# Optimization experiments

Measured on AMD Instinct MI355X. Metric: run time of the kernel, lower is better.

Reference implementation:

```python
import jax, jax.numpy as jnp
import numpy as np

N_NODES = 100000


def _mean_agg(x, src, dst, n_nodes):
    # gather source features along edges, segment-sum into destinations, divide by in-degree
    msg = x[src]                                               # [E, D]
    s = jax.ops.segment_sum(msg, dst, num_segments=n_nodes)    # [N, D]
    deg = jax.ops.segment_sum(jnp.ones((src.shape[0],), x.dtype), dst, num_segments=n_nodes)
    return s / jnp.maximum(deg, 1.0)[:, None]


def _sage_layer(x, src, dst, W_self, W_neigh, b, n_nodes):
    h_neigh = _mean_agg(x, src, dst, n_nodes)
    return x @ W_self + h_neigh @ W_neigh + b


def setup_inputs() -> dict:
    key = jax.random.key(0)
    ks = jax.random.split(key, 8)
    in_f, h_f, n_cls = 128, 128, 40
    n_edges = 1600000
    sc = lambda d: 1.0 / np.sqrt(d)
    return {
        "features": jax.random.normal(ks[0], (N_NODES, in_f), dtype=jnp.float32),
        "src": jax.random.randint(ks[1], (n_edges,), 0, N_NODES),
        "dst": jax.random.randint(ks[2], (n_edges,), 0, N_NODES),
        "W1_self": jax.random.normal(ks[3], (in_f, h_f), dtype=jnp.float32) * sc(in_f),
        "W1_neigh": jax.random.normal(ks[4], (in_f, h_f), dtype=jnp.float32) * sc(in_f),
        "b1": jnp.zeros((h_f,), dtype=jnp.float32),
        "W2_self": jax.random.normal(ks[5], (h_f, n_cls), dtype=jnp.float32) * sc(h_f),
        "W2_neigh": jax.random.normal(ks[6], (h_f, n_cls), dtype=jnp.float32) * sc(h_f),
        "b2": jnp.zeros((n_cls,), dtype=jnp.float32),
    }


def reference(features, src, dst, W1_self, W1_neigh, b1, W2_self, W2_neigh, b2):
    h = _sage_layer(features, src, dst, W1_self, W1_neigh, b1, N_NODES)
    h = jax.nn.relu(h)
    h = _sage_layer(h, src, dst, W2_self, W2_neigh, b2, N_NODES)
    return h
```

## Files before the change

kernel.cpp:

```cpp
#include <hip/hip_runtime.h>


typedef __attribute__((ext_vector_type(8))) short bf16x8;
typedef __attribute__((ext_vector_type(4))) float f32x4;
typedef __attribute__((ext_vector_type(2))) float f32x2;

#define BIN_SHIFT 7
#define BIN_SIZE  128
#define NB        256

#define OFF_ROWSTART (1ull << 20)
#define OFF_HIST     (2ull << 20)
#define OFF_SCAN     (3ull << 20)
#define OFF_BSUMS    (4ull << 20)
#define OFF_BOFFS    ((4ull << 20) + (64ull << 10))
#define OFF_PACKED   (5ull << 20)
#define OFF_CSR      (12ull << 20)
#define OFF_W1T      (19ull << 20)
#define OFF_W2T      (20ull << 20)
#define OFF_XB       (21ull << 20)
#define OFF_XQ       (47ull << 20)
#define OFF_AGGB     (61ull << 20)
#define OFF_T2LO     (87ull << 20)
#define OFF_T2HI     (94ull << 20)

static __device__ __forceinline__ unsigned short f2b(float f) {
    unsigned int u = __float_as_uint(f);
    u += 0x7fffu + ((u >> 16) & 1u);
    return (unsigned short)(u >> 16);
}
static __device__ __forceinline__ float blo(unsigned int v) { return __uint_as_float(v << 16); }
static __device__ __forceinline__ float bhi(unsigned int v) { return __uint_as_float(v & 0xffff0000u); }


__global__ __launch_bounds__(256) void hist_local(
    const int* __restrict__ dst, int* __restrict__ hist, int E, int nbins) {
    __shared__ int h[1024];
    int b = blockIdx.x, t = threadIdx.x;
    for (int i = t; i < nbins; i += 256) h[i] = 0;
    __syncthreads();
    int chunk = (E + NB - 1) / NB;
    int base = b * chunk;
    int lim = min(base + chunk, E);
    for (int e = base + t; e < lim; e += 256)
        atomicAdd(&h[dst[e] >> BIN_SHIFT], 1);
    __syncthreads();
    for (int i = t; i < nbins; i += 256)
        hist[i * NB + b] = h[i];
}

__global__ void scan1(const int* __restrict__ in, int* __restrict__ tmp,
                      int* __restrict__ bsums, int M) {
    __shared__ int s[256];
    int t = threadIdx.x;
    int i = blockIdx.x * 256 + t;
    int v = (i < M) ? in[i] : 0;
    s[t] = v;
    __syncthreads();
    for (int off = 1; off < 256; off <<= 1) {
        int u = (t >= off) ? s[t - off] : 0;
        __syncthreads();
        s[t] += u;
        __syncthreads();
    }
    if (i < M) tmp[i] = s[t] - v;
    if (t == 255) bsums[blockIdx.x] = s[t];
}

__global__ void scan2(const int* __restrict__ bsums, int* __restrict__ boffs, int nb) {
    __shared__ int s[1024];
    int t = threadIdx.x;
    int v = (t < nb) ? bsums[t] : 0;
    s[t] = v;
    __syncthreads();
    for (int off = 1; off < 1024; off <<= 1) {
        int u = (t >= off) ? s[t - off] : 0;
        __syncthreads();
        s[t] += u;
        __syncthreads();
    }
    if (t < nb) boffs[t] = s[t] - v;
}

__global__ __launch_bounds__(256) void scatter_det(
    const int* __restrict__ src, const int* __restrict__ dst,
    const int* __restrict__ tmp, const int* __restrict__ boffs,
    unsigned int* __restrict__ packed, int E, int nbins) {
    __shared__ int cur[1024];
    int b = blockIdx.x, t = threadIdx.x;
    for (int i = t; i < nbins; i += 256) cur[i] = tmp[i * NB + b] + boffs[i];
    __syncthreads();
    int chunk = (E + NB - 1) / NB;
    int base = b * chunk;
    int lim = min(base + chunk, E);
    for (int e = base + t; e < lim; e += 256) {
        int d = dst[e];
        int bin = d >> BIN_SHIFT;
        int pos = atomicAdd(&cur[bin], 1);
        packed[pos] = ((unsigned int)(d & (BIN_SIZE - 1)) << 20) | (unsigned int)src[e];
    }
}

__global__ __launch_bounds__(256) void bin_fill(
    const unsigned int* __restrict__ packed, const int* __restrict__ tmp,
    const int* __restrict__ boffs,
    int* __restrict__ row_start, int* __restrict__ csr_src, int N, int nbins, int E) {
    __shared__ int cnt[BIN_SIZE];
    __shared__ int pre[BIN_SIZE];
    __shared__ int ex[BIN_SIZE];
    int b = blockIdx.x;
    int t = threadIdx.x;
    int node0 = b << BIN_SHIFT;
    int beg = tmp[b * NB] + boffs[b];
    int end = (b + 1 < nbins) ? (tmp[(b + 1) * NB] + boffs[b + 1]) : E;

    if (t < BIN_SIZE) cnt[t] = 0;
    __syncthreads();
    for (int i = beg + t; i < end; i += 256)
        atomicAdd(&cnt[packed[i] >> 20], 1);
    __syncthreads();
    if (t < BIN_SIZE) pre[t] = cnt[t];
    __syncthreads();
    for (int off = 1; off < BIN_SIZE; off <<= 1) {
        int u = (t < BIN_SIZE && t >= off) ? pre[t - off] : 0;
        __syncthreads();
        if (t < BIN_SIZE) pre[t] += u;
        __syncthreads();
    }
    if (t < BIN_SIZE) {
        ex[t] = pre[t] - cnt[t];
        int node = node0 + t;
        if (node < N) row_start[node] = beg + ex[t];
        cnt[t] = 0;
    }
    if (b == nbins - 1 && t == 0) row_start[N] = E;
    __syncthreads();
    for (int i = beg + t; i < end; i += 256) {
        unsigned int p = packed[i];
        int dl = p >> 20;
        int s = p & 0xFFFFF;
        int ofs = atomicAdd(&cnt[dl], 1);
        csr_src[beg + ex[dl] + ofs] = s;
    }
}


__global__ void cast_prep(const float* __restrict__ x,
                          const float* __restrict__ W1s, const float* __restrict__ W1n,
                          const float* __restrict__ W2s, const float* __restrict__ W2n,
                          unsigned short* __restrict__ xb, unsigned char* __restrict__ xq,
                          unsigned short* __restrict__ W1t, unsigned short* __restrict__ W2t,
                          unsigned short* __restrict__ t2lo, unsigned short* __restrict__ t2hi,
                          int n16, int castBlocks, int N) {
    int blk = blockIdx.x, t = threadIdx.x;
    if (blk < castBlocks) {
        int i = blk * 256 + t;
        if (i >= n16) return;
        const float4* p = (const float4*)x + (size_t)i * 4;
        float4 v0 = p[0], v1 = p[1], v2 = p[2], v3 = p[3];
        float f[16] = {v0.x, v0.y, v0.z, v0.w, v1.x, v1.y, v1.z, v1.w,
                       v2.x, v2.y, v2.z, v2.w, v3.x, v3.y, v3.z, v3.w};
        unsigned short ob[16];
#pragma unroll
        for (int k = 0; k < 16; k++) ob[k] = f2b(f[k]);
        *(float4*)(xb + (size_t)i * 16) = *(float4*)&ob[0];
        *(float4*)(xb + (size_t)i * 16 + 8) = *(float4*)&ob[8];
        unsigned int w[4];
#pragma unroll
        for (int k = 0; k < 4; k++) {
            int u = __builtin_amdgcn_cvt_pk_fp8_f32(f[4 * k + 0], f[4 * k + 1], 0, false);
            u = __builtin_amdgcn_cvt_pk_fp8_f32(f[4 * k + 2], f[4 * k + 3], u, true);
            w[k] = (unsigned int)u;
        }
        *(uint4*)(xq + (size_t)i * 16) = *(uint4*)w;
    } else if (blk < castBlocks + 128) {
        int c = blk - castBlocks;
        float v = (t < 128) ? W1s[(size_t)t * 128 + c] : W1n[(size_t)(t - 128) * 128 + c];
        W1t[(size_t)c * 256 + t] = f2b(v);
    } else if (blk < castBlocks + 208) {
        if (t < 128) {
            int c = blk - castBlocks - 128;
            float v = (c < 40) ? W2s[(size_t)t * 40 + c] : W2n[(size_t)t * 40 + (c - 40)];
            W2t[(size_t)c * 128 + t] = f2b(v);
        }
    } else {
        if (t < 32) ((unsigned int*)(xq + (size_t)N * 128))[t] = 0u;
        else if (t < 48) ((unsigned int*)(t2lo + (size_t)N * 32))[t - 32] = 0u;
        else if (t < 52) ((unsigned int*)(t2hi + (size_t)N * 8))[t - 48] = 0u;
    }
}


__global__ void agg_mean_fp8(const unsigned char* __restrict__ xq,
                             const int* __restrict__ row_start,
                             const int* __restrict__ csr_src,
                             unsigned short* __restrict__ aggb, int N) {
    int wave = (blockIdx.x * blockDim.x + threadIdx.x) >> 6;
    int lane = threadIdx.x & 63;
    if (wave >= N) return;
    int q = lane >> 4;
    int l = lane & 15;
    int beg = row_start[wave], end = row_start[wave + 1];
    const char* xbase = (const char*)xq;
    unsigned loff = (unsigned)l << 3;

    float a[8];
#pragma unroll
    for (int k = 0; k < 8; k++) a[k] = 0.f;

    for (int e = beg; e < end; e += 16) {
        int eq = e + 4 * q;
        int s[4];
#pragma unroll
        for (int k = 0; k < 4; k++) {
            int ee = eq + k;
            int idx = csr_src[min(ee, end - 1)];
            s[k] = (ee < end) ? idx : N;
        }
#pragma unroll
        for (int k = 0; k < 4; k++) {
            uint2 v = *(const uint2*)(xbase + (((unsigned)s[k] << 7) + loff));
            f32x2 p0 = __builtin_amdgcn_cvt_pk_f32_fp8(v.x, false);
            f32x2 p1 = __builtin_amdgcn_cvt_pk_f32_fp8(v.x, true);
            f32x2 p2 = __builtin_amdgcn_cvt_pk_f32_fp8(v.y, false);
            f32x2 p3 = __builtin_amdgcn_cvt_pk_f32_fp8(v.y, true);
            a[0] += p0.x; a[1] += p0.y; a[2] += p1.x; a[3] += p1.y;
            a[4] += p2.x; a[5] += p2.y; a[6] += p3.x; a[7] += p3.y;
        }
    }

#pragma unroll
    for (int k = 0; k < 8; k++) {
        a[k] += __shfl_xor(a[k], 16);
        a[k] += __shfl_xor(a[k], 32);
    }
    if (q == 0) {
        float inv = 1.0f / fmaxf((float)(end - beg), 1.0f);
        unsigned int ow[4];
#pragma unroll
        for (int k = 0; k < 4; k++)
            ow[k] = (unsigned int)f2b(a[2 * k] * inv) |
                    ((unsigned int)f2b(a[2 * k + 1] * inv) << 16);
        *(uint4*)((char*)aggb + (((unsigned)wave << 8) + ((unsigned)l << 4))) = *(uint4*)ow;
    }
}

__global__ void agg2_add(const unsigned short* __restrict__ t2lo,
                         const unsigned short* __restrict__ t2hi,
                         const int* __restrict__ row_start,
                         const int* __restrict__ csr_src, const float* __restrict__ b2,
                         float* __restrict__ out, int N) {
    int wave = (blockIdx.x * blockDim.x + threadIdx.x) >> 6;
    int lane = threadIdx.x & 63;
    if (wave >= N) return;
    int q = lane >> 4;
    int l = lane & 15;
    int beg = row_start[wave], end = row_start[wave + 1];
    const char* lob = (const char*)t2lo;
    const char* hib = (const char*)t2hi;
    bool isLo = (l < 8);
    bool active = (l < 10);
    unsigned loff = isLo ? ((unsigned)l << 3) : ((unsigned)(l - 8) << 3);

    float a0 = 0.f, a1 = 0.f, a2 = 0.f, a3 = 0.f;

    for (int e = beg; e < end; e += 16) {
        int eq = e + 4 * q;
        int s[4];
#pragma unroll
        for (int k = 0; k < 4; k++) {
            int ee = eq + k;
            int idx = csr_src[min(ee, end - 1)];
            s[k] = (ee < end) ? idx : N;
        }
        if (active) {
#pragma unroll
            for (int k = 0; k < 4; k++) {
                uint2 v = isLo ? *(const uint2*)(lob + (((unsigned)s[k] << 6) + loff))
                               : *(const uint2*)(hib + (((unsigned)s[k] << 4) + loff));
                a0 += blo(v.x); a1 += bhi(v.x);
                a2 += blo(v.y); a3 += bhi(v.y);
            }
        }
    }

    a0 += __shfl_xor(a0, 16); a0 += __shfl_xor(a0, 32);
    a1 += __shfl_xor(a1, 16); a1 += __shfl_xor(a1, 32);
    a2 += __shfl_xor(a2, 16); a2 += __shfl_xor(a2, 32);
    a3 += __shfl_xor(a3, 16); a3 += __shfl_xor(a3, 32);
    if (q == 0 && active) {
        float inv = 1.0f / fmaxf((float)(end - beg), 1.0f);
        float4 bb = ((const float4*)b2)[l];
        float4* op = (float4*)((char*)out + ((unsigned)wave * 160u + ((unsigned)l << 4)));
        float4 cur = *op;
        cur.x += a0 * inv + bb.x;
        cur.y += a1 * inv + bb.y;
        cur.z += a2 * inv + bb.z;
        cur.w += a3 * inv + bb.w;
        *op = cur;
    }
}


__global__ __launch_bounds__(256) void gemm12_mfma(
    const unsigned short* __restrict__ xb, const unsigned short* __restrict__ aggb,
    const unsigned short* __restrict__ W1t, const unsigned short* __restrict__ W2t,
    const float* __restrict__ b1, float* __restrict__ out,
    unsigned short* __restrict__ t2lo, unsigned short* __restrict__ t2hi, int N) {

    __shared__ unsigned short As[128 * 40];
    __shared__ unsigned short Bs[128 * 40];
    __shared__ unsigned short Hs[128 * 136];
    __shared__ unsigned short B2[80 * 136];

    int tid = threadIdx.x;
    int wave = tid >> 6, lane = tid & 63;
    int row0 = blockIdx.x * 128;
    int m = lane & 15, quad = lane >> 4;

    for (int idx = tid; idx < 1280; idx += 256) {
        int r = idx >> 4, seg = idx & 15;
        *(float4*)&B2[r * 136 + seg * 8] = *(const float4*)(W2t + (size_t)r * 128 + seg * 8);
    }

    f32x4 acc[2][8];
#pragma unroll
    for (int i = 0; i < 2; i++)
#pragma unroll
        for (int j = 0; j < 8; j++) acc[i][j] = (f32x4){0.f, 0.f, 0.f, 0.f};

    for (int k0 = 0; k0 < 256; k0 += 32) {
        __syncthreads();
        {
            int r = tid >> 1, kk = (tid & 1) * 16;
            int row = row0 + r;
            float4 v0 = make_float4(0, 0, 0, 0), v1 = v0;
            if (row < N) {
                const unsigned short* s = (k0 < 128)
                    ? (xb + (size_t)row * 128 + k0 + kk)
                    : (aggb + (size_t)row * 128 + (k0 - 128) + kk);
                const float4* p = (const float4*)s;
                v0 = p[0]; v1 = p[1];
            }
            *(float4*)&As[r * 40 + kk] = v0;
            *(float4*)&As[r * 40 + kk + 8] = v1;
            const float4* q2 = (const float4*)(W1t + (size_t)r * 256 + k0 + kk);
            float4 w0 = q2[0], w1 = q2[1];
            *(float4*)&Bs[r * 40 + kk] = w0;
            *(float4*)&Bs[r * 40 + kk + 8] = w1;
        }
        __syncthreads();

        bf16x8 af0 = *(bf16x8*)&As[(wave * 32 + m) * 40 + quad * 8];
        bf16x8 af1 = *(bf16x8*)&As[(wave * 32 + 16 + m) * 40 + quad * 8];
#pragma unroll
        for (int j = 0; j < 8; j++) {
            bf16x8 bfg = *(bf16x8*)&Bs[(j * 16 + m) * 40 + quad * 8];
            acc[0][j] = __builtin_amdgcn_mfma_f32_16x16x32_bf16(af0, bfg, acc[0][j], 0, 0, 0);
            acc[1][j] = __builtin_amdgcn_mfma_f32_16x16x32_bf16(af1, bfg, acc[1][j], 0, 0, 0);
        }
    }

#pragma unroll
    for (int j = 0; j < 8; j++) {
        int col = j * 16 + m;
        float bias = b1[col];
#pragma unroll
        for (int i = 0; i < 2; i++) {
#pragma unroll
            for (int r = 0; r < 4; r++) {
                int rl = wave * 32 + i * 16 + quad * 4 + r;
                Hs[rl * 136 + col] = f2b(fmaxf(acc[i][j][r] + bias, 0.f));
            }
        }
    }
    __syncthreads();

    f32x4 acc2[2][5];
#pragma unroll
    for (int i = 0; i < 2; i++)
#pragma unroll
        for (int j = 0; j < 5; j++) acc2[i][j] = (f32x4){0.f, 0.f, 0.f, 0.f};

#pragma unroll
    for (int k0 = 0; k0 < 128; k0 += 32) {
        bf16x8 af0 = *(bf16x8*)&Hs[(wave * 32 + m) * 136 + k0 + quad * 8];
        bf16x8 af1 = *(bf16x8*)&Hs[(wave * 32 + 16 + m) * 136 + k0 + quad * 8];
#pragma unroll
        for (int j = 0; j < 5; j++) {
            bf16x8 bfg = *(bf16x8*)&B2[(j * 16 + m) * 136 + k0 + quad * 8];
            acc2[0][j] = __builtin_amdgcn_mfma_f32_16x16x32_bf16(af0, bfg, acc2[0][j], 0, 0, 0);
            acc2[1][j] = __builtin_amdgcn_mfma_f32_16x16x32_bf16(af1, bfg, acc2[1][j], 0, 0, 0);
        }
    }

#pragma unroll
    for (int j = 0; j < 5; j++) {
        int col = j * 16 + m;
#pragma unroll
        for (int i = 0; i < 2; i++) {
#pragma unroll
            for (int r = 0; r < 4; r++) {
                int row = row0 + wave * 32 + i * 16 + quad * 4 + r;
                if (row < N) {
                    float v = acc2[i][j][r];
                    if (col < 40) {
                        out[(size_t)row * 40 + col] = v;
                    } else {
                        int td = col - 40;
                        if (td < 32) t2lo[(size_t)row * 32 + td] = f2b(v);
                        else         t2hi[(size_t)row * 8 + (td - 32)] = f2b(v);
                    }
                }
            }
        }
    }
}


extern "C" void kernel_launch(void* const* d_in, const int* in_sizes, int n_in,
                              void* d_out, int out_size, void* d_ws, size_t ws_size,
                              hipStream_t stream) {
    const float* x   = (const float*)d_in[0];
    const int*   src = (const int*)d_in[1];
    const int*   dst = (const int*)d_in[2];
    const float* W1s = (const float*)d_in[3];
    const float* W1n = (const float*)d_in[4];
    const float* b1  = (const float*)d_in[5];
    const float* W2s = (const float*)d_in[6];
    const float* W2n = (const float*)d_in[7];
    const float* b2  = (const float*)d_in[8];
    float* out = (float*)d_out;

    int N = in_sizes[0] / 128;
    int E = in_sizes[1];
    int nbins = (N + BIN_SIZE - 1) / BIN_SIZE;
    int M = nbins * NB;

    char* ws = (char*)d_ws;
    int*            row_start  = (int*)(ws + OFF_ROWSTART);
    int*            hist       = (int*)(ws + OFF_HIST);
    int*            scanned    = (int*)(ws + OFF_SCAN);
    int*            bsums      = (int*)(ws + OFF_BSUMS);
    int*            boffs      = (int*)(ws + OFF_BOFFS);
    unsigned int*   packed     = (unsigned int*)(ws + OFF_PACKED);
    int*            csr_src    = (int*)(ws + OFF_CSR);
    unsigned short* W1t        = (unsigned short*)(ws + OFF_W1T);
    unsigned short* W2t        = (unsigned short*)(ws + OFF_W2T);
    unsigned short* xb         = (unsigned short*)(ws + OFF_XB);
    unsigned char*  xq         = (unsigned char*)(ws + OFF_XQ);
    unsigned short* aggb       = (unsigned short*)(ws + OFF_AGGB);
    unsigned short* t2lo       = (unsigned short*)(ws + OFF_T2LO);
    unsigned short* t2hi       = (unsigned short*)(ws + OFF_T2HI);

    int scanBlocks = (M + 255) / 256;

    hist_local<<<NB, 256, 0, stream>>>(dst, hist, E, nbins);
    scan1<<<scanBlocks, 256, 0, stream>>>(hist, scanned, bsums, M);
    scan2<<<1, 1024, 0, stream>>>(bsums, boffs, scanBlocks);
    scatter_det<<<NB, 256, 0, stream>>>(src, dst, scanned, boffs, packed, E, nbins);
    bin_fill<<<nbins, 256, 0, stream>>>(packed, scanned, boffs, row_start, csr_src, N, nbins, E);

    int n16 = N * 128 / 16;
    int castBlocks = (n16 + 255) / 256;
    cast_prep<<<castBlocks + 128 + 80 + 1, 256, 0, stream>>>(
        x, W1s, W1n, W2s, W2n, xb, xq, W1t, W2t, t2lo, t2hi, n16, castBlocks, N);

    int aggBlocks = (N * 64 + 255) / 256;
    agg_mean_fp8<<<aggBlocks, 256, 0, stream>>>(xq, row_start, csr_src, aggb, N);
    gemm12_mfma<<<(N + 127) / 128, 256, 0, stream>>>(xb, aggb, W1t, W2t, b1, out, t2lo, t2hi, N);
    agg2_add<<<aggBlocks, 256, 0, stream>>>(t2lo, t2hi, row_start, csr_src, b2, out, N);
}
```

Measured before the change: 276.2 us.

## Split second-layer aggregation into two column halves to shrink gather footprint

The 40-column layer-2 neighbor table is now stored as two 20-column bf16 halves, 40 bytes per row each, instead of a 32+8 split. The aggregation kernel runs twice as many blocks, and each block gathers only one half. Blocks are interleaved in groups of four so both halves of nearby nodes run close together in time, which keeps each half table small enough to stay cache resident. The CSR index loads and the output read-modify-write also become nontemporal. The cost is that every edge's index list is read twice and the per-lane gathers shrink to 4 bytes.

Measured after the change: 327.3 us. +18.5%, slower.

```diff
diff --git a/kernel.cpp b/kernel.cpp
--- a/kernel.cpp
+++ b/kernel.cpp
@@ -21,8 +21,8 @@
 #define OFF_XB       (21ull << 20)
 #define OFF_XQ       (47ull << 20)
 #define OFF_AGGB     (61ull << 20)
-#define OFF_T2LO     (87ull << 20)
-#define OFF_T2HI     (94ull << 20)
+#define OFF_T2A      (87ull << 20)
+#define OFF_T2B      (91ull << 20)
 
 static __device__ __forceinline__ unsigned short f2b(float f) {
     unsigned int u = __float_as_uint(f);
@@ -150,7 +150,7 @@
                           const float* __restrict__ W2s, const float* __restrict__ W2n,
                           unsigned short* __restrict__ xb, unsigned char* __restrict__ xq,
                           unsigned short* __restrict__ W1t, unsigned short* __restrict__ W2t,
-                          unsigned short* __restrict__ t2lo, unsigned short* __restrict__ t2hi,
+                          unsigned short* __restrict__ t2a, unsigned short* __restrict__ t2b,
                           int n16, int castBlocks, int N) {
     int blk = blockIdx.x, t = threadIdx.x;
     if (blk < castBlocks) {
@@ -185,8 +185,8 @@
         }
     } else {
         if (t < 32) ((unsigned int*)(xq + (size_t)N * 128))[t] = 0u;
-        else if (t < 48) ((unsigned int*)(t2lo + (size_t)N * 32))[t - 32] = 0u;
-        else if (t < 52) ((unsigned int*)(t2hi + (size_t)N * 8))[t - 48] = 0u;
+        else if (t < 42) ((unsigned int*)((char*)t2a + (size_t)N * 40))[t - 32] = 0u;
+        else if (t < 52) ((unsigned int*)((char*)t2b + (size_t)N * 40))[t - 42] = 0u;
     }
 }
 
@@ -245,24 +245,25 @@
     }
 }
 
-__global__ void agg2_add(const unsigned short* __restrict__ t2lo,
-                         const unsigned short* __restrict__ t2hi,
-                         const int* __restrict__ row_start,
-                         const int* __restrict__ csr_src, const float* __restrict__ b2,
-                         float* __restrict__ out, int N) {
-    int wave = (blockIdx.x * blockDim.x + threadIdx.x) >> 6;
+__global__ void agg2_split(const unsigned short* __restrict__ t2a,
+                           const unsigned short* __restrict__ t2b,
+                           const int* __restrict__ row_start,
+                           const int* __restrict__ csr_src, const float* __restrict__ b2,
+                           float* __restrict__ out, int N) {
+    int bid = blockIdx.x;
+    int h = (bid >> 2) & 1;
+    int nb = ((bid >> 3) << 2) | (bid & 3);
+    int node = nb * 4 + (threadIdx.x >> 6);
+    if (node >= N) return;
     int lane = threadIdx.x & 63;
-    if (wave >= N) return;
     int q = lane >> 4;
     int l = lane & 15;
-    int beg = row_start[wave], end = row_start[wave + 1];
-    const char* lob = (const char*)t2lo;
-    const char* hib = (const char*)t2hi;
-    bool isLo = (l < 8);
+    int beg = row_start[node], end = row_start[node + 1];
+    const char* tb = h ? (const char*)t2b : (const char*)t2a;
     bool active = (l < 10);
-    unsigned loff = isLo ? ((unsigned)l << 3) : ((unsigned)(l - 8) << 3);
-
-    float a0 = 0.f, a1 = 0.f, a2 = 0.f, a3 = 0.f;
+    unsigned loff = (unsigned)l << 2;
+
+    float a0 = 0.f, a1 = 0.f;
 
     for (int e = beg; e < end; e += 16) {
         int eq = e + 4 * q;
@@ -270,34 +271,29 @@
 #pragma unroll
         for (int k = 0; k < 4; k++) {
             int ee = eq + k;
-            int idx = csr_src[min(ee, end - 1)];
+            int idx = __builtin_nontemporal_load(csr_src + min(ee, end - 1));
             s[k] = (ee < end) ? idx : N;
         }
         if (active) {
 #pragma unroll
             for (int k = 0; k < 4; k++) {
-                uint2 v = isLo ? *(const uint2*)(lob + (((unsigned)s[k] << 6) + loff))
-                               : *(const uint2*)(hib + (((unsigned)s[k] << 4) + loff));
-                a0 += blo(v.x); a1 += bhi(v.x);
-                a2 += blo(v.y); a3 += bhi(v.y);
+                unsigned int v = *(const unsigned int*)(tb + ((unsigned)s[k] * 40u + loff));
+                a0 += blo(v); a1 += bhi(v);
             }
         }
     }
 
     a0 += __shfl_xor(a0, 16); a0 += __shfl_xor(a0, 32);
     a1 += __shfl_xor(a1, 16); a1 += __shfl_xor(a1, 32);
-    a2 += __shfl_xor(a2, 16); a2 += __shfl_xor(a2, 32);
-    a3 += __shfl_xor(a3, 16); a3 += __shfl_xor(a3, 32);
     if (q == 0 && active) {
         float inv = 1.0f / fmaxf((float)(end - beg), 1.0f);
-        float4 bb = ((const float4*)b2)[l];
-        float4* op = (float4*)((char*)out + ((unsigned)wave * 160u + ((unsigned)l << 4)));
-        float4 cur = *op;
-        cur.x += a0 * inv + bb.x;
-        cur.y += a1 * inv + bb.y;
-        cur.z += a2 * inv + bb.z;
-        cur.w += a3 * inv + bb.w;
-        *op = cur;
+        const float* bp = b2 + h * 20 + l * 2;
+        f32x2* op = (f32x2*)((char*)out + ((size_t)node * 160u + (unsigned)h * 80u + ((unsigned)l << 3)));
+        f32x2 cur = __builtin_nontemporal_load(op);
+        f32x2 nv;
+        nv.x = cur.x + a0 * inv + bp[0];
+        nv.y = cur.y + a1 * inv + bp[1];
+        __builtin_nontemporal_store(nv, op);
     }
 }
 
@@ -306,7 +302,7 @@
     const unsigned short* __restrict__ xb, const unsigned short* __restrict__ aggb,
     const unsigned short* __restrict__ W1t, const unsigned short* __restrict__ W2t,
     const float* __restrict__ b1, float* __restrict__ out,
-    unsigned short* __restrict__ t2lo, unsigned short* __restrict__ t2hi, int N) {
+    unsigned short* __restrict__ t2a, unsigned short* __restrict__ t2b, int N) {
 
     __shared__ unsigned short As[128 * 40];
     __shared__ unsigned short Bs[128 * 40];
@@ -408,8 +404,9 @@
                         out[(size_t)row * 40 + col] = v;
                     } else {
                         int td = col - 40;
-                        if (td < 32) t2lo[(size_t)row * 32 + td] = f2b(v);
-                        else         t2hi[(size_t)row * 8 + (td - 32)] = f2b(v);
+                        unsigned short hv = f2b(v);
+                        if (td < 20) t2a[(size_t)row * 20 + td] = hv;
+                        else         t2b[(size_t)row * 20 + (td - 20)] = hv;
                     }
                 }
             }
@@ -450,8 +447,8 @@
     unsigned short* xb         = (unsigned short*)(ws + OFF_XB);
     unsigned char*  xq         = (unsigned char*)(ws + OFF_XQ);
     unsigned short* aggb       = (unsigned short*)(ws + OFF_AGGB);
-    unsigned short* t2lo       = (unsigned short*)(ws + OFF_T2LO);
-    unsigned short* t2hi       = (unsigned short*)(ws + OFF_T2HI);
+    unsigned short* t2a        = (unsigned short*)(ws + OFF_T2A);
+    unsigned short* t2b        = (unsigned short*)(ws + OFF_T2B);
 
     int scanBlocks = (M + 255) / 256;
 
@@ -464,10 +461,13 @@
     int n16 = N * 128 / 16;
     int castBlocks = (n16 + 255) / 256;
     cast_prep<<<castBlocks + 128 + 80 + 1, 256, 0, stream>>>(
-        x, W1s, W1n, W2s, W2n, xb, xq, W1t, W2t, t2lo, t2hi, n16, castBlocks, N);
+        x, W1s, W1n, W2s, W2n, xb, xq, W1t, W2t, t2a, t2b, n16, castBlocks, N);
 
     int aggBlocks = (N * 64 + 255) / 256;
     agg_mean_fp8<<<aggBlocks, 256, 0, stream>>>(xq, row_start, csr_src, aggb, N);
-    gemm12_mfma<<<(N + 127) / 128, 256, 0, stream>>>(xb, aggb, W1t, W2t, b1, out, t2lo, t2hi, N);
-    agg2_add<<<aggBlocks, 256, 0, stream>>>(t2lo, t2hi, row_start, csr_src, b2, out, N);
-}
+    gemm12_mfma<<<(N + 127) / 128, 256, 0, stream>>>(xb, aggb, W1t, W2t, b1, out, t2a, t2b, N);
+
+    int B0 = (N + 3) / 4;
+    int blocks2 = ((2 * B0 + 7) / 8) * 8;
+    agg2_split<<<blocks2, 256, 0, stream>>>(t2a, t2b, row_start, csr_src, b2, out, N);
+}
```

## Replace per-node CSR layer-2 aggregation with bin-wise LDS atomic accumulation

Applied to the files above, without the earlier changes.

The second-layer neighbor aggregation no longer uses one wave per destination node walking CSR. Each block now owns a 128-node bin and streams that bin's packed (dst_local, src) edges, gathering bf16 rows of the projected features and accumulating them with shared-memory float atomics. It then scales by inverse degree and adds into the output. The b2 bias add moves into the GEMM epilogue and the sentinel zero-row writes are dropped. This aims to remove low lane utilization and per-node index reads, at the cost of LDS atomic contention and a nondeterministic summation order.

Result: slower. 674.4 us (+144.2%).

```diff
diff --git a/kernel.cpp b/kernel.cpp
--- a/kernel.cpp
+++ b/kernel.cpp
@@ -23,6 +23,7 @@
 #define OFF_AGGB     (61ull << 20)
 #define OFF_T2LO     (87ull << 20)
 #define OFF_T2HI     (94ull << 20)
+#define T2HI_DELTA   (7u << 20)
 
 static __device__ __forceinline__ unsigned short f2b(float f) {
     unsigned int u = __float_as_uint(f);
@@ -150,7 +151,6 @@
                           const float* __restrict__ W2s, const float* __restrict__ W2n,
                           unsigned short* __restrict__ xb, unsigned char* __restrict__ xq,
                           unsigned short* __restrict__ W1t, unsigned short* __restrict__ W2t,
-                          unsigned short* __restrict__ t2lo, unsigned short* __restrict__ t2hi,
                           int n16, int castBlocks, int N) {
     int blk = blockIdx.x, t = threadIdx.x;
     if (blk < castBlocks) {
@@ -185,8 +185,6 @@
         }
     } else {
         if (t < 32) ((unsigned int*)(xq + (size_t)N * 128))[t] = 0u;
-        else if (t < 48) ((unsigned int*)(t2lo + (size_t)N * 32))[t - 32] = 0u;
-        else if (t < 52) ((unsigned int*)(t2hi + (size_t)N * 8))[t - 48] = 0u;
     }
 }
 
@@ -245,59 +243,64 @@
     }
 }
 
-__global__ void agg2_add(const unsigned short* __restrict__ t2lo,
-                         const unsigned short* __restrict__ t2hi,
-                         const int* __restrict__ row_start,
-                         const int* __restrict__ csr_src, const float* __restrict__ b2,
-                         float* __restrict__ out, int N) {
-    int wave = (blockIdx.x * blockDim.x + threadIdx.x) >> 6;
-    int lane = threadIdx.x & 63;
-    if (wave >= N) return;
-    int q = lane >> 4;
-    int l = lane & 15;
-    int beg = row_start[wave], end = row_start[wave + 1];
-    const char* lob = (const char*)t2lo;
-    const char* hib = (const char*)t2hi;
-    bool isLo = (l < 8);
-    bool active = (l < 10);
-    unsigned loff = isLo ? ((unsigned)l << 3) : ((unsigned)(l - 8) << 3);
-
-    float a0 = 0.f, a1 = 0.f, a2 = 0.f, a3 = 0.f;
-
-    for (int e = beg; e < end; e += 16) {
-        int eq = e + 4 * q;
-        int s[4];
-#pragma unroll
-        for (int k = 0; k < 4; k++) {
-            int ee = eq + k;
-            int idx = csr_src[min(ee, end - 1)];
-            s[k] = (ee < end) ? idx : N;
-        }
-        if (active) {
-#pragma unroll
-            for (int k = 0; k < 4; k++) {
-                uint2 v = isLo ? *(const uint2*)(lob + (((unsigned)s[k] << 6) + loff))
-                               : *(const uint2*)(hib + (((unsigned)s[k] << 4) + loff));
-                a0 += blo(v.x); a1 += bhi(v.x);
-                a2 += blo(v.y); a3 += bhi(v.y);
-            }
-        }
-    }
-
-    a0 += __shfl_xor(a0, 16); a0 += __shfl_xor(a0, 32);
-    a1 += __shfl_xor(a1, 16); a1 += __shfl_xor(a1, 32);
-    a2 += __shfl_xor(a2, 16); a2 += __shfl_xor(a2, 32);
-    a3 += __shfl_xor(a3, 16); a3 += __shfl_xor(a3, 32);
-    if (q == 0 && active) {
-        float inv = 1.0f / fmaxf((float)(end - beg), 1.0f);
-        float4 bb = ((const float4*)b2)[l];
-        float4* op = (float4*)((char*)out + ((unsigned)wave * 160u + ((unsigned)l << 4)));
-        float4 cur = *op;
-        cur.x += a0 * inv + bb.x;
-        cur.y += a1 * inv + bb.y;
-        cur.z += a2 * inv + bb.z;
-        cur.w += a3 * inv + bb.w;
-        *op = cur;
+__global__ __launch_bounds__(512) void agg2_bin(
+    const unsigned short* __restrict__ t2lo,
+    const unsigned int* __restrict__ packed,
+    const int* __restrict__ row_start,
+    float* __restrict__ out, int N) {
+
+    __shared__ float accf[128 * 44];
+    __shared__ float sinv[128];
+
+    int tid = threadIdx.x;
+    int b = blockIdx.x;
+    int node0 = b << BIN_SHIFT;
+
+    for (int i = tid; i < 128 * 44; i += 512) accf[i] = 0.f;
+    if (tid < 128) {
+        int node = node0 + tid;
+        int dg = (node < N) ? row_start[node + 1] - row_start[node] : 1;
+        sinv[tid] = 1.0f / (float)max(dg, 1);
+    }
+    int beg = row_start[node0];
+    int end = row_start[min(node0 + BIN_SIZE, N)];
+    __syncthreads();
+
+    int wave = tid >> 6, lane = tid & 63;
+    int eslot = lane / 10;
+    int dslot = lane - eslot * 10;
+    bool isLo = (dslot < 8);
+    unsigned shiftv = isLo ? 6u : 4u;
+    unsigned addv = isLo ? ((unsigned)dslot << 3)
+                         : (T2HI_DELTA + ((unsigned)(dslot - 8) << 3));
+    bool act = (eslot < 6);
+    const char* t2b = (const char*)t2lo;
+
+#pragma unroll 2
+    for (int ew = beg + wave * 6; ew < end; ew += 48) {
+        int ee = ew + eslot;
+        if (act && ee < end) {
+            unsigned p = packed[ee];
+            int dl = (int)(p >> 20);
+            unsigned s = p & 0xFFFFFu;
+            uint2 v = *(const uint2*)(t2b + ((s << shiftv) + addv));
+            float* ap = accf + dl * 44 + (dslot << 2);
+            atomicAdd(ap + 0, blo(v.x));
+            atomicAdd(ap + 1, bhi(v.x));
+            atomicAdd(ap + 2, blo(v.y));
+            atomicAdd(ap + 3, bhi(v.y));
+        }
+    }
+    __syncthreads();
+
+    for (int idx = tid; idx < 128 * 40; idx += 512) {
+        int n = idx / 40;
+        int d = idx - n * 40;
+        int node = node0 + n;
+        if (node < N) {
+            float* op = out + (size_t)node * 40 + d;
+            *op += accf[n * 44 + d] * sinv[n];
+        }
     }
 }
 
@@ -305,7 +308,8 @@
 __global__ __launch_bounds__(256) void gemm12_mfma(
     const unsigned short* __restrict__ xb, const unsigned short* __restrict__ aggb,
     const unsigned short* __restrict__ W1t, const unsigned short* __restrict__ W2t,
-    const float* __restrict__ b1, float* __restrict__ out,
+    const float* __restrict__ b1, const float* __restrict__ b2,
+    float* __restrict__ out,
     unsigned short* __restrict__ t2lo, unsigned short* __restrict__ t2hi, int N) {
 
     __shared__ unsigned short As[128 * 40];
@@ -397,6 +401,7 @@
 #pragma unroll
     for (int j = 0; j < 5; j++) {
         int col = j * 16 + m;
+        float b2v = (col < 40) ? b2[col] : 0.f;
 #pragma unroll
         for (int i = 0; i < 2; i++) {
 #pragma unroll
@@ -405,7 +410,7 @@
                 if (row < N) {
                     float v = acc2[i][j][r];
                     if (col < 40) {
-                        out[(size_t)row * 40 + col] = v;
+                        out[(size_t)row * 40 + col] = v + b2v;
                     } else {
                         int td = col - 40;
                         if (td < 32) t2lo[(size_t)row * 32 + td] = f2b(v);
@@ -464,10 +469,11 @@
     int n16 = N * 128 / 16;
     int castBlocks = (n16 + 255) / 256;
     cast_prep<<<castBlocks + 128 + 80 + 1, 256, 0, stream>>>(
-        x, W1s, W1n, W2s, W2n, xb, xq, W1t, W2t, t2lo, t2hi, n16, castBlocks, N);
+        x, W1s, W1n, W2s, W2n, xb, xq, W1t, W2t, n16, castBlocks, N);
 
     int aggBlocks = (N * 64 + 255) / 256;
     agg_mean_fp8<<<aggBlocks, 256, 0, stream>>>(xq, row_start, csr_src, aggb, N);
-    gemm12_mfma<<<(N + 127) / 128, 256, 0, stream>>>(xb, aggb, W1t, W2t, b1, out, t2lo, t2hi, N);
-    agg2_add<<<aggBlocks, 256, 0, stream>>>(t2lo, t2hi, row_start, csr_src, b2, out, N);
-}
+    gemm12_mfma<<<(N + 127) / 128, 256, 0, stream>>>(xb, aggb, W1t, W2t, b1, b2, out, t2lo, t2hi, N);
+
+    agg2_bin<<<nbins, 512, 0, stream>>>(t2lo, packed, row_start, out, N);
+}
```

## Map two nodes per wave in aggregation kernels and fuse cast with histogram

Applied to the files above, without the earlier changes.

The two neighbor-aggregation kernels now give each 32-lane half-wave its own destination node, with 16 lanes per edge stream and 8 edges per lane per iteration, where before one full wave handled a single node. This halves the number of waves and drops one shuffle-reduction stage, aimed at the low per-node work of average degree about 16. Separately, the feature/weight cast kernel and the dst histogram kernel are merged into one launch to save a launch and let the two overlap. The cost is more divergence when the two nodes in a wave have very different degrees, and more registers for the 8-way index array.

Result: no change. 273.9 us, median of 2 (-0.8%).

```diff
diff --git a/kernel.cpp b/kernel.cpp
--- a/kernel.cpp
+++ b/kernel.cpp
@@ -33,21 +33,68 @@
 static __device__ __forceinline__ float bhi(unsigned int v) { return __uint_as_float(v & 0xffff0000u); }
 
 
-__global__ __launch_bounds__(256) void hist_local(
-    const int* __restrict__ dst, int* __restrict__ hist, int E, int nbins) {
+__global__ __launch_bounds__(256) void cast_hist(
+    const float* __restrict__ x,
+    const float* __restrict__ W1s, const float* __restrict__ W1n,
+    const float* __restrict__ W2s, const float* __restrict__ W2n,
+    unsigned short* __restrict__ xb, unsigned char* __restrict__ xq,
+    unsigned short* __restrict__ W1t, unsigned short* __restrict__ W2t,
+    unsigned short* __restrict__ t2lo, unsigned short* __restrict__ t2hi,
+    const int* __restrict__ dst, int* __restrict__ hist,
+    int n16, int castBlocks, int castPlus, int N, int E, int nbins) {
     __shared__ int h[1024];
-    int b = blockIdx.x, t = threadIdx.x;
-    for (int i = t; i < nbins; i += 256) h[i] = 0;
-    __syncthreads();
-    int chunk = (E + NB - 1) / NB;
-    int base = b * chunk;
-    int lim = min(base + chunk, E);
-    for (int e = base + t; e < lim; e += 256)
-        atomicAdd(&h[dst[e] >> BIN_SHIFT], 1);
-    __syncthreads();
-    for (int i = t; i < nbins; i += 256)
-        hist[i * NB + b] = h[i];
-}
+    int blk = blockIdx.x, t = threadIdx.x;
+    if (blk >= castPlus) {
+        int b = blk - castPlus;
+        for (int i = t; i < nbins; i += 256) h[i] = 0;
+        __syncthreads();
+        int chunk = (E + NB - 1) / NB;
+        int base = b * chunk;
+        int lim = min(base + chunk, E);
+        for (int e = base + t; e < lim; e += 256)
+            atomicAdd(&h[dst[e] >> BIN_SHIFT], 1);
+        __syncthreads();
+        for (int i = t; i < nbins; i += 256)
+            hist[i * NB + b] = h[i];
+        return;
+    }
+    if (blk < castBlocks) {
+        int i = blk * 256 + t;
+        if (i >= n16) return;
+        const float4* p = (const float4*)x + (size_t)i * 4;
+        float4 v0 = p[0], v1 = p[1], v2 = p[2], v3 = p[3];
+        float f[16] = {v0.x, v0.y, v0.z, v0.w, v1.x, v1.y, v1.z, v1.w,
+                       v2.x, v2.y, v2.z, v2.w, v3.x, v3.y, v3.z, v3.w};
+        unsigned short ob[16];
+#pragma unroll
+        for (int k = 0; k < 16; k++) ob[k] = f2b(f[k]);
+        *(float4*)(xb + (size_t)i * 16) = *(float4*)&ob[0];
+        *(float4*)(xb + (size_t)i * 16 + 8) = *(float4*)&ob[8];
+        unsigned int w[4];
+#pragma unroll
+        for (int k = 0; k < 4; k++) {
+            int u = __builtin_amdgcn_cvt_pk_fp8_f32(f[4 * k + 0], f[4 * k + 1], 0, false);
+            u = __builtin_amdgcn_cvt_pk_fp8_f32(f[4 * k + 2], f[4 * k + 3], u, true);
+            w[k] = (unsigned int)u;
+        }
+        *(uint4*)(xq + (size_t)i * 16) = *(uint4*)w;
+    } else if (blk < castBlocks + 128) {
+        int c = blk - castBlocks;
+        float v = (t < 128) ? W1s[(size_t)t * 128 + c] : W1n[(size_t)(t - 128) * 128 + c];
+        W1t[(size_t)c * 256 + t] = f2b(v);
+    } else if (blk < castBlocks + 208) {
+        if (t < 128) {
+            int c = blk - castBlocks - 128;
+            float v = (c < 40) ? W2s[(size_t)t * 40 + c] : W2n[(size_t)t * 40 + (c - 40)];
+            W2t[(size_t)c * 128 + t] = f2b(v);
+        }
+    } else {
+        if (t < 32) ((unsigned int*)(xq + (size_t)N * 128))[t] = 0u;
+        else if (t < 48) ((unsigned int*)(t2lo + (size_t)N * 32))[t - 32] = 0u;
+        else if (t < 52) ((unsigned int*)(t2hi + (size_t)N * 8))[t - 48] = 0u;
+    }
+}
+
 
 __global__ void scan1(const int* __restrict__ in, int* __restrict__ tmp,
                       int* __restrict__ bsums, int M) {
@@ -145,62 +192,20 @@
 }
 
 
-__global__ void cast_prep(const float* __restrict__ x,
-                          const float* __restrict__ W1s, const float* __restrict__ W1n,
-                          const float* __restrict__ W2s, const float* __restrict__ W2n,
-                          unsigned short* __restrict__ xb, unsigned char* __restrict__ xq,
-                          unsigned short* __restrict__ W1t, unsigned short* __restrict__ W2t,
-                          unsigned short* __restrict__ t2lo, unsigned short* __restrict__ t2hi,
-                          int n16, int castBlocks, int N) {
-    int blk = blockIdx.x, t = threadIdx.x;
-    if (blk < castBlocks) {
-        int i = blk * 256 + t;
-        if (i >= n16) return;
-        const float4* p = (const float4*)x + (size_t)i * 4;
-        float4 v0 = p[0], v1 = p[1], v2 = p[2], v3 = p[3];
-        float f[16] = {v0.x, v0.y, v0.z, v0.w, v1.x, v1.y, v1.z, v1.w,
-                       v2.x, v2.y, v2.z, v2.w, v3.x, v3.y, v3.z, v3.w};
-        unsigned short ob[16];
-#pragma unroll
-        for (int k = 0; k < 16; k++) ob[k] = f2b(f[k]);
-        *(float4*)(xb + (size_t)i * 16) = *(float4*)&ob[0];
-        *(float4*)(xb + (size_t)i * 16 + 8) = *(float4*)&ob[8];
-        unsigned int w[4];
-#pragma unroll
-        for (int k = 0; k < 4; k++) {
-            int u = __builtin_amdgcn_cvt_pk_fp8_f32(f[4 * k + 0], f[4 * k + 1], 0, false);
-            u = __builtin_amdgcn_cvt_pk_fp8_f32(f[4 * k + 2], f[4 * k + 3], u, true);
-            w[k] = (unsigned int)u;
-        }
-        *(uint4*)(xq + (size_t)i * 16) = *(uint4*)w;
-    } else if (blk < castBlocks + 128) {
-        int c = blk - castBlocks;
-        float v = (t < 128) ? W1s[(size_t)t * 128 + c] : W1n[(size_t)(t - 128) * 128 + c];
-        W1t[(size_t)c * 256 + t] = f2b(v);
-    } else if (blk < castBlocks + 208) {
-        if (t < 128) {
-            int c = blk - castBlocks - 128;
-            float v = (c < 40) ? W2s[(size_t)t * 40 + c] : W2n[(size_t)t * 40 + (c - 40)];
-            W2t[(size_t)c * 128 + t] = f2b(v);
-        }
-    } else {
-        if (t < 32) ((unsigned int*)(xq + (size_t)N * 128))[t] = 0u;
-        else if (t < 48) ((unsigned int*)(t2lo + (size_t)N * 32))[t - 32] = 0u;
-        else if (t < 52) ((unsigned int*)(t2hi + (size_t)N * 8))[t - 48] = 0u;
-    }
-}
-
-
 __global__ void agg_mean_fp8(const unsigned char* __restrict__ xq,
                              const int* __restrict__ row_start,
                              const int* __restrict__ csr_src,
                              unsigned short* __restrict__ aggb, int N) {
-    int wave = (blockIdx.x * blockDim.x + threadIdx.x) >> 6;
+    int wv = (blockIdx.x * blockDim.x + threadIdx.x) >> 6;
     int lane = threadIdx.x & 63;
-    if (wave >= N) return;
-    int q = lane >> 4;
-    int l = lane & 15;
-    int beg = row_start[wave], end = row_start[wave + 1];
+    if (2 * wv >= N) return;
+    int node = 2 * wv + (lane >> 5);
+    bool valid = node < N;
+    int hl = lane & 31;
+    int g = hl >> 4;
+    int l = hl & 15;
+    int beg = valid ? row_start[node] : 0;
+    int end = valid ? row_start[node + 1] : 0;
     const char* xbase = (const char*)xq;
     unsigned loff = (unsigned)l << 3;
 
@@ -209,16 +214,15 @@
     for (int k = 0; k < 8; k++) a[k] = 0.f;
 
     for (int e = beg; e < end; e += 16) {
-        int eq = e + 4 * q;
-        int s[4];
-#pragma unroll
-        for (int k = 0; k < 4; k++) {
-            int ee = eq + k;
+        int s[8];
+#pragma unroll
+        for (int k = 0; k < 8; k++) {
+            int ee = e + 2 * k + g;
             int idx = csr_src[min(ee, end - 1)];
             s[k] = (ee < end) ? idx : N;
         }
 #pragma unroll
-        for (int k = 0; k < 4; k++) {
+        for (int k = 0; k < 8; k++) {
             uint2 v = *(const uint2*)(xbase + (((unsigned)s[k] << 7) + loff));
             f32x2 p0 = __builtin_amdgcn_cvt_pk_f32_fp8(v.x, false);
             f32x2 p1 = __builtin_amdgcn_cvt_pk_f32_fp8(v.x, true);
@@ -230,18 +234,16 @@
     }
 
 #pragma unroll
-    for (int k = 0; k < 8; k++) {
+    for (int k = 0; k < 8; k++)
         a[k] += __shfl_xor(a[k], 16);
-        a[k] += __shfl_xor(a[k], 32);
-    }
-    if (q == 0) {
+    if (g == 0 && valid) {
         float inv = 1.0f / fmaxf((float)(end - beg), 1.0f);
         unsigned int ow[4];
 #pragma unroll
         for (int k = 0; k < 4; k++)
             ow[k] = (unsigned int)f2b(a[2 * k] * inv) |
                     ((unsigned int)f2b(a[2 * k + 1] * inv) << 16);
-        *(uint4*)((char*)aggb + (((unsigned)wave << 8) + ((unsigned)l << 4))) = *(uint4*)ow;
+        *(uint4*)((char*)aggb + (((unsigned)node << 8) + ((unsigned)l << 4))) = *(uint4*)ow;
     }
 }
 
@@ -250,12 +252,16 @@
                          const int* __restrict__ row_start,
                          const int* __restrict__ csr_src, const float* __restrict__ b2,
                          float* __restrict__ out, int N) {
-    int wave = (blockIdx.x * blockDim.x + threadIdx.x) >> 6;
+    int wv = (blockIdx.x * blockDim.x + threadIdx.x) >> 6;
     int lane = threadIdx.x & 63;
-    if (wave >= N) return;
-    int q = lane >> 4;
-    int l = lane & 15;
-    int beg = row_start[wave], end = row_start[wave + 1];
+    if (2 * wv >= N) return;
+    int node = 2 * wv + (lane >> 5);
+    bool valid = node < N;
+    int hl = lane & 31;
+    int g = hl >> 4;
+    int l = hl & 15;
+    int beg = valid ? row_start[node] : 0;
+    int end = valid ? row_start[node + 1] : 0;
     const char* lob = (const char*)t2lo;
     const char* hib = (const char*)t2hi;
     bool isLo = (l < 8);
@@ -265,17 +271,16 @@
     float a0 = 0.f, a1 = 0.f, a2 = 0.f, a3 = 0.f;
 
     for (int e = beg; e < end; e += 16) {
-        int eq = e + 4 * q;
-        int s[4];
-#pragma unroll
-        for (int k = 0; k < 4; k++) {
-            int ee = eq + k;
+        int s[8];
+#pragma unroll
+        for (int k = 0; k < 8; k++) {
+            int ee = e + 2 * k + g;
             int idx = csr_src[min(ee, end - 1)];
             s[k] = (ee < end) ? idx : N;
         }
         if (active) {
 #pragma unroll
-            for (int k = 0; k < 4; k++) {
+            for (int k = 0; k < 8; k++) {
                 uint2 v = isLo ? *(const uint2*)(lob + (((unsigned)s[k] << 6) + loff))
                                : *(const uint2*)(hib + (((unsigned)s[k] << 4) + loff));
                 a0 += blo(v.x); a1 += bhi(v.x);
@@ -284,14 +289,14 @@
         }
     }
 
-    a0 += __shfl_xor(a0, 16); a0 += __shfl_xor(a0, 32);
-    a1 += __shfl_xor(a1, 16); a1 += __shfl_xor(a1, 32);
-    a2 += __shfl_xor(a2, 16); a2 += __shfl_xor(a2, 32);
-    a3 += __shfl_xor(a3, 16); a3 += __shfl_xor(a3, 32);
-    if (q == 0 && active) {
+    a0 += __shfl_xor(a0, 16);
+    a1 += __shfl_xor(a1, 16);
+    a2 += __shfl_xor(a2, 16);
+    a3 += __shfl_xor(a3, 16);
+    if (g == 0 && active && valid) {
         float inv = 1.0f / fmaxf((float)(end - beg), 1.0f);
         float4 bb = ((const float4*)b2)[l];
-        float4* op = (float4*)((char*)out + ((unsigned)wave * 160u + ((unsigned)l << 4)));
+        float4* op = (float4*)((char*)out + ((unsigned)node * 160u + ((unsigned)l << 4)));
         float4 cur = *op;
         cur.x += a0 * inv + bb.x;
         cur.y += a1 * inv + bb.y;
@@ -455,18 +460,20 @@
 
     int scanBlocks = (M + 255) / 256;
 
-    hist_local<<<NB, 256, 0, stream>>>(dst, hist, E, nbins);
+    int n16 = N * 128 / 16;
+    int castBlocks = (n16 + 255) / 256;
+    int castPlus = castBlocks + 128 + 80 + 1;
+
+    cast_hist<<<castPlus + NB, 256, 0, stream>>>(
+        x, W1s, W1n, W2s, W2n, xb, xq, W1t, W2t, t2lo, t2hi,
+        dst, hist, n16, castBlocks, castPlus, N, E, nbins);
     scan1<<<scanBlocks, 256, 0, stream>>>(hist, scanned, bsums, M);
     scan2<<<1, 1024, 0, stream>>>(bsums, boffs, scanBlocks);
     scatter_det<<<NB, 256, 0, stream>>>(src, dst, scanned, boffs, packed, E, nbins);
     bin_fill<<<nbins, 256, 0, stream>>>(packed, scanned, boffs, row_start, csr_src, N, nbins, E);
 
-    int n16 = N * 128 / 16;
-    int castBlocks = (n16 + 255) / 256;
-    cast_prep<<<castBlocks + 128 + 80 + 1, 256, 0, stream>>>(
-        x, W1s, W1n, W2s, W2n, xb, xq, W1t, W2t, t2lo, t2hi, n16, castBlocks, N);
-
-    int aggBlocks = (N * 64 + 255) / 256;
+    int nodePairs = (N + 1) / 2;
+    int aggBlocks = (nodePairs * 64 + 255) / 256;
     agg_mean_fp8<<<aggBlocks, 256, 0, stream>>>(xq, row_start, csr_src, aggb, N);
     gemm12_mfma<<<(N + 127) / 128, 256, 0, stream>>>(xb, aggb, W1t, W2t, b1, out, t2lo, t2hi, N);
     agg2_add<<<aggBlocks, 256, 0, stream>>>(t2lo, t2hi, row_start, csr_src, b2, out, N);
```
